# Kernel tuning notes

Hardware: AMD Instinct MI355X
Metric: run time of the kernel (lower is better)

The kernel has to match this reference:

```python
import jax, jax.numpy as jnp
import numpy as np
from jax import lax

VOCAB = 32000
EMBED = 300
HIDDEN = 1024
BATCH = 64
SEQLEN = 512


def setup_inputs() -> dict:
    key = jax.random.key(0)
    k1, k2, k3, k4 = jax.random.split(key, 4)
    seq = jax.random.randint(k1, (BATCH, SEQLEN), 0, VOCAB, dtype=jnp.int32)
    embedding_table = jax.random.normal(k2, (VOCAB, EMBED), dtype=jnp.float32) * 0.1
    # Keras LSTM params: kernel [E, 4H], recurrent_kernel [H, 4H], bias [4H]; gate order i,f,c,o
    kernel = jax.random.normal(k3, (EMBED, 4 * HIDDEN), dtype=jnp.float32) * (1.0 / np.sqrt(EMBED))
    recurrent_kernel = jax.random.normal(k4, (HIDDEN, 4 * HIDDEN), dtype=jnp.float32) * (1.0 / np.sqrt(HIDDEN))
    # Keras unit_forget_bias default: forget-gate bias = 1
    bias = jnp.concatenate([
        jnp.zeros((HIDDEN,), jnp.float32),
        jnp.ones((HIDDEN,), jnp.float32),
        jnp.zeros((2 * HIDDEN,), jnp.float32),
    ])
    return {"embedding_table": embedding_table, "kernel": kernel,
            "recurrent_kernel": recurrent_kernel, "bias": bias, "seq": seq}


def _masked_lstm(x, mask, kernel, recurrent_kernel, bias):
    # x: [B,T,E], mask: [B,T] bool. Returns final hidden state [B,H].
    B = x.shape[0]
    H = recurrent_kernel.shape[0]
    # precompute input projections for all steps: [T,B,4H]
    xz = jnp.einsum('bte,eg->tbg', x, kernel) + bias
    mask_t = mask.T  # [T,B]

    def step(carry, inp):
        h, c = carry
        zx, mt = inp  # zx [B,4H], mt [B]
        z = zx + h @ recurrent_kernel
        zi, zf, zg, zo = jnp.split(z, 4, axis=-1)
        i = jax.nn.sigmoid(zi)
        f = jax.nn.sigmoid(zf)
        g = jnp.tanh(zg)
        o = jax.nn.sigmoid(zo)
        c_new = f * c + i * g
        h_new = o * jnp.tanh(c_new)
        m = mt[:, None]
        h = jnp.where(m, h_new, h)
        c = jnp.where(m, c_new, c)
        return (h, c), None

    h0 = jnp.zeros((B, H), x.dtype)
    c0 = jnp.zeros((B, H), x.dtype)
    (h, _), _ = lax.scan(step, (h0, c0), (xz, mask_t))
    return h


def reference(embedding_table, kernel, recurrent_kernel, bias, seq):
    x = embedding_table[seq]          # [B,T,E] embedding lookup
    mask = seq != 0                   # mask_zero=True: token id 0 is padding
    return _masked_lstm(x, mask, kernel, recurrent_kernel, bias)
```

## Files before the change

### kernel.cpp

```cpp
#include <hip/hip_runtime.h>

#define TT 512
#define BB 64
#define EE 300
#define HH 1024
#define GG 4096
#define NSLOT 33

typedef _Float16 f16x8 __attribute__((ext_vector_type(8)));
typedef float f32x4 __attribute__((ext_vector_type(4)));


__device__ __forceinline__ float sigmf(float x) {
    return __fdividef(1.0f, 1.0f + __expf(-x));
}
__device__ __forceinline__ float tanhsf(float x) {
    float e = __expf(-2.0f * fabsf(x));
    float r = __fdividef(1.0f - e, 1.0f + e);
    return copysignf(r, x);
}

__global__ void mask_kernel(const int* __restrict__ seq, float* __restrict__ maskf) {
    int idx = blockIdx.x * 256 + threadIdx.x;
    int t = idx >> 6, b = idx & 63;
    maskf[idx] = (seq[b * TT + t] != 0) ? 1.0f : 0.0f;
}

__global__ __launch_bounds__(256)
void xgather_kernel(const float* __restrict__ emb, const int* __restrict__ seq,
                    _Float16* __restrict__ xA) {
    __shared__ float xrow[64 * 305];
    const int t = blockIdx.x, tid = threadIdx.x;
    const int r = tid >> 2, sub = tid & 3;
    const int row = seq[r * TT + t];
    for (int e = sub; e < EE; e += 4)
        xrow[r * 305 + e] = emb[row * EE + e];
    __syncthreads();
    unsigned int* dst = (unsigned int*)(xA + (size_t)t * 20480);
    for (int idx = tid; idx < 10240; idx += 256) {
        int el = idx << 1;
        int j = el & 7, b = (el >> 3) & 63, quad = (el >> 9) & 3, kb = el >> 11;
        int e = (kb << 5) + (quad << 3) + j;
        union { _Float16 h[2]; unsigned int u; } pk;
        pk.h[0] = (e < EE)     ? (_Float16)xrow[b * 305 + e]     : (_Float16)0.f;
        pk.h[1] = (e + 1 < EE) ? (_Float16)xrow[b * 305 + e + 1] : (_Float16)0.f;
        dst[idx] = pk.u;
    }
}

__global__ __launch_bounds__(512, 2)
void lstm_kernel(const _Float16* __restrict__ xA, const float* __restrict__ rk,
                 const float* __restrict__ wk, const float* __restrict__ bias,
                 const float* __restrict__ maskf, _Float16* __restrict__ hbuf,
                 unsigned int* __restrict__ flags, float* __restrict__ out) {
    __shared__ _Float16 RbL[16384];
    __shared__ _Float16 WbL[5120];
    __shared__ float zb[8704];
    __shared__ float cs[2048];
    __shared__ _Float16 hshh[256];
    const int tid = threadIdx.x;
    const int lane = tid & 63;
    const int w = tid >> 6;
    const int p = blockIdx.x;
    const int p4 = p << 2;
    const int cc = lane & 15, quad = lane >> 4;

    for (int i = tid; i < 16384; i += 512) {
        int k = i >> 4, c = i & 15;
        float v = rk[k * GG + ((c >> 2) << 10) + p4 + (c & 3)];
        RbL[((k >> 5) << 9) + (((k >> 3) & 3) << 7) + (c << 3) + (k & 7)] = (_Float16)v;
    }
    for (int i = tid; i < 5120; i += 512) {
        int e = i >> 4, c = i & 15;
        float v = (e < EE) ? wk[e * GG + ((c >> 2) << 10) + p4 + (c & 3)] : 0.f;
        WbL[((e >> 5) << 9) + (((e >> 3) & 3) << 7) + (c << 3) + (e & 7)] = (_Float16)v;
    }
    if (tid < 256) cs[tid] = 0.f;
    float bb[4];
    if (w < 4) {
#pragma unroll
        for (int gt = 0; gt < 4; ++gt)
            bb[gt] = bias[(gt << 10) + p4 + w];
    }
    int slot = 0, nslot = 1;
    float hown = 0.0f;
    const int fidx = (w << 5) + (lane & 31);
    const f16x8* RbH = (const f16x8*)RbL;
    const f16x8* WbH = (const f16x8*)WbL;
    __syncthreads();

    for (int t = 0; t < TT; ++t) {
        float m = maskf[(t << 6) + lane];
        f32x4 acc[4];
#pragma unroll
        for (int mt = 0; mt < 4; ++mt) acc[mt] = (f32x4){0.f, 0.f, 0.f, 0.f};

        const f16x8* xA8 = (const f16x8*)(xA + (size_t)t * 20480);
        {
            int kb = w;
            f16x8 bf = WbH[(kb << 6) + (quad << 4) + cc];
#pragma unroll
            for (int mt = 0; mt < 4; ++mt) {
                f16x8 af = xA8[(kb << 8) + (quad << 6) + (mt << 4) + cc];
                acc[mt] = __builtin_amdgcn_mfma_f32_16x16x32_f16(af, bf, acc[mt], 0, 0, 0);
            }
        }
        if (w < 2) {
            int kb = 8 + w;
            f16x8 bf = WbH[(kb << 6) + (quad << 4) + cc];
#pragma unroll
            for (int mt = 0; mt < 4; ++mt) {
                f16x8 af = xA8[(kb << 8) + (quad << 6) + (mt << 4) + cc];
                acc[mt] = __builtin_amdgcn_mfma_f32_16x16x32_f16(af, bf, acc[mt], 0, 0, 0);
            }
        }

        if (t > 0) {
            unsigned int tgt = (unsigned int)t;
            while (!__all((int)(__hip_atomic_load(flags + fidx, __ATOMIC_RELAXED,
                                                  __HIP_MEMORY_SCOPE_AGENT) >= tgt)))
                __builtin_amdgcn_s_sleep(1);
        }
        __builtin_amdgcn_sched_barrier(0);

        const f16x8* hA8 = (const f16x8*)(hbuf + (size_t)slot * 65536);
#pragma unroll
        for (int kc = 0; kc < 4; ++kc) {
            int kb = (w << 2) + kc;
            f16x8 bf = RbH[(kb << 6) + (quad << 4) + cc];
#pragma unroll
            for (int mt = 0; mt < 4; ++mt) {
                f16x8 af = hA8[(kb << 8) + (quad << 6) + (mt << 4) + cc];
                acc[mt] = __builtin_amdgcn_mfma_f32_16x16x32_f16(af, bf, acc[mt], 0, 0, 0);
            }
        }
#pragma unroll
        for (int mt = 0; mt < 4; ++mt)
            *(f32x4*)(zb + ((w << 4) + cc) * 68 + (mt << 4) + (quad << 2)) = acc[mt];
        __syncthreads();
        if (w < 4) {
            float z[4];
#pragma unroll
            for (int gt = 0; gt < 4; ++gt) {
                int c = (gt << 2) + w;
                float s = bb[gt];
#pragma unroll
                for (int wp = 0; wp < 8; ++wp) s += zb[((wp << 4) + c) * 68 + lane];
                z[gt] = s;
            }
            float fi = sigmf(z[0]);
            float ff = sigmf(z[1]);
            float fg = tanhsf(z[2]);
            float fo = sigmf(z[3]);
            float co = cs[(w << 6) + lane];
            float cn = fmaf(ff, co, fi * fg);
            cn = fmaf(m, cn - co, co);
            cs[(w << 6) + lane] = cn;
            float hc = fo * tanhsf(cn);
            hown = fmaf(m, hc - hown, hown);
            hshh[(lane << 2) + w] = (_Float16)hown;
        }
        __syncthreads();
        if (tid < 64) {
            unsigned long long hv = ((const unsigned long long*)hshh)[lane];
            size_t el = (size_t)nslot * 65536 + ((size_t)(p >> 3) << 11) +
                        ((size_t)((p >> 1) & 3) << 9) + (lane << 3) + ((p & 1) << 2);
            __hip_atomic_store((unsigned long long*)(hbuf + el), hv,
                               __ATOMIC_RELAXED, __HIP_MEMORY_SCOPE_AGENT);
        }
        __syncthreads();
        if (tid == 0)
            __hip_atomic_store(flags + p, (unsigned int)(t + 1),
                               __ATOMIC_RELAXED, __HIP_MEMORY_SCOPE_AGENT);
        slot = nslot;
        nslot = (nslot + 1 == NSLOT) ? 0 : nslot + 1;
    }
    if (w < 4) zb[(w << 6) + lane] = hown;
    __syncthreads();
    if (tid < 64) {
        float4 v = make_float4(zb[tid], zb[64 + tid], zb[128 + tid], zb[192 + tid]);
        *(float4*)(out + tid * HH + p4) = v;
    }
}

extern "C" void kernel_launch(void* const* d_in, const int* in_sizes, int n_in,
                              void* d_out, int out_size, void* d_ws, size_t ws_size,
                              hipStream_t stream) {
    const float* emb  = (const float*)d_in[0];
    const float* wk   = (const float*)d_in[1];
    const float* rk   = (const float*)d_in[2];
    const float* bias = (const float*)d_in[3];
    const int*   seq  = (const int*)d_in[4];
    float* out = (float*)d_out;
    char* ws = (char*)d_ws;

    const size_t off_hbuf = 1024;
    const size_t off_mask = off_hbuf + (size_t)NSLOT * 131072;
    const size_t off_xA   = off_mask + 131072;
    unsigned int* flags = (unsigned int*)ws;
    _Float16* hbuf  = (_Float16*)(ws + off_hbuf);
    float*    maskf = (float*)(ws + off_mask);
    _Float16* xA    = (_Float16*)(ws + off_xA);

    hipMemsetAsync(ws, 0, off_hbuf + 131072, stream);
    mask_kernel<<<128, 256, 0, stream>>>(seq, maskf);
    xgather_kernel<<<TT, 256, 0, stream>>>(emb, seq, xA);
    lstm_kernel<<<256, 512, 0, stream>>>(xA, rk, wk, bias, maskf, hbuf, flags, out);
}
```

Baseline: 1.880 ms.

## Warp-specialize LSTM step into producer MFMA warps and consumer gate warp pipelined per batch group

Each step is split across waves. Seven waves compute MFMA partial sums for one 16-row batch group at a time, and one dedicated wave reduces them, applies the gate nonlinearities and publishes h. Block-wide __syncthreads are replaced by per-wave progress counters in LDS and a double-buffered z buffer, so gate math for one group overlaps the matmul for the next. The recurrent and input weight fragments are hoisted into registers, and the xA and hbuf layouts are changed to group-major. A dummy padding shared array, touched only behind an impossible pointer check, forces LDS usage, which looks aimed at limiting occupancy. The change adds spin-wait complexity and the risk of ordering bugs.

```diff
diff --git a/kernel.cpp b/kernel.cpp
--- a/kernel.cpp
+++ b/kernel.cpp
@@ -39,11 +39,13 @@
     unsigned int* dst = (unsigned int*)(xA + (size_t)t * 20480);
     for (int idx = tid; idx < 10240; idx += 256) {
         int el = idx << 1;
-        int j = el & 7, b = (el >> 3) & 63, quad = (el >> 9) & 3, kb = el >> 11;
+        int j = el & 7, b = (el >> 3) & 15, quad = (el >> 7) & 3, r2 = el >> 9;
+        int g = r2 / 10, kb = r2 - g * 10;
         int e = (kb << 5) + (quad << 3) + j;
+        int bg = (g << 4) + b;
         union { _Float16 h[2]; unsigned int u; } pk;
-        pk.h[0] = (e < EE)     ? (_Float16)xrow[b * 305 + e]     : (_Float16)0.f;
-        pk.h[1] = (e + 1 < EE) ? (_Float16)xrow[b * 305 + e + 1] : (_Float16)0.f;
+        pk.h[0] = (e < EE)     ? (_Float16)xrow[bg * 305 + e]     : (_Float16)0.f;
+        pk.h[1] = (e + 1 < EE) ? (_Float16)xrow[bg * 305 + e + 1] : (_Float16)0.f;
         dst[idx] = pk.u;
     }
 }
@@ -55,9 +57,12 @@
                  unsigned int* __restrict__ flags, float* __restrict__ out) {
     __shared__ _Float16 RbL[16384];
     __shared__ _Float16 WbL[5120];
-    __shared__ float zb[8704];
-    __shared__ float cs[2048];
-    __shared__ _Float16 hshh[256];
+    __shared__ float zb[4480];
+    __shared__ float cs[256];
+    __shared__ __align__(8) _Float16 hsh[64];
+    __shared__ unsigned int prog[8];
+    __shared__ unsigned int rel;
+    __shared__ float padf[6200];
     const int tid = threadIdx.x;
     const int lane = tid & 63;
     const int w = tid >> 6;
@@ -76,110 +81,125 @@
         WbL[((e >> 5) << 9) + (((e >> 3) & 3) << 7) + (c << 3) + (e & 7)] = (_Float16)v;
     }
     if (tid < 256) cs[tid] = 0.f;
-    float bb[4];
-    if (w < 4) {
-#pragma unroll
-        for (int gt = 0; gt < 4; ++gt)
-            bb[gt] = bias[(gt << 10) + p4 + w];
-    }
-    int slot = 0, nslot = 1;
-    float hown = 0.0f;
-    const int fidx = (w << 5) + (lane & 31);
-    const f16x8* RbH = (const f16x8*)RbL;
-    const f16x8* WbH = (const f16x8*)WbL;
+    if (tid < 8) prog[tid] = (tid == 7) ? 0xFFFFFFFFu : 0u;
+    if (tid == 0) rel = 0u;
     __syncthreads();
-
-    for (int t = 0; t < TT; ++t) {
-        float m = maskf[(t << 6) + lane];
-        f32x4 acc[4];
-#pragma unroll
-        for (int mt = 0; mt < 4; ++mt) acc[mt] = (f32x4){0.f, 0.f, 0.f, 0.f};
-
-        const f16x8* xA8 = (const f16x8*)(xA + (size_t)t * 20480);
-        {
-            int kb = w;
-            f16x8 bf = WbH[(kb << 6) + (quad << 4) + cc];
-#pragma unroll
-            for (int mt = 0; mt < 4; ++mt) {
-                f16x8 af = xA8[(kb << 8) + (quad << 6) + (mt << 4) + cc];
-                acc[mt] = __builtin_amdgcn_mfma_f32_16x16x32_f16(af, bf, acc[mt], 0, 0, 0);
+    if ((size_t)out == 1) { padf[tid] = cs[0]; out[0] = padf[tid]; }
+
+    if (w == 0) {
+        const int uu = lane >> 4, b = lane & 15;
+        float bb0 = bias[p4 + uu], bb1 = bias[1024 + p4 + uu];
+        float bb2 = bias[2048 + p4 + uu], bb3 = bias[3072 + p4 + uu];
+        float hw[4] = {0.f, 0.f, 0.f, 0.f};
+        const size_t puboff = ((((size_t)(p >> 3) << 2) + ((p >> 1) & 3)) << 7)
+                              + ((size_t)lane << 3) + ((size_t)(p & 1) << 2);
+        for (int t = 0; t < TT; ++t) {
+            _Float16* hb = hbuf + (size_t)((t + 1) % NSLOT) * 65536;
+#pragma unroll
+            for (int g = 0; g < 4; ++g) {
+                const int id = (t << 2) + g;
+                while (!__all((int)(__hip_atomic_load(prog + (lane & 7), __ATOMIC_ACQUIRE,
+                                                      __HIP_MEMORY_SCOPE_WORKGROUP)
+                                    >= (unsigned)(id + 1))))
+                    __builtin_amdgcn_s_sleep(0);
+                __builtin_amdgcn_sched_barrier(0);
+                const float* zr = zb + (id & 1) * 2240;
+                float z0 = bb0, z1 = bb1, z2 = bb2, z3 = bb3;
+#pragma unroll
+                for (int wp = 0; wp < 7; ++wp) {
+                    const float* zw = zr + (wp << 4) * 20;
+                    z0 += zw[uu * 20 + b];
+                    z1 += zw[(4 + uu) * 20 + b];
+                    z2 += zw[(8 + uu) * 20 + b];
+                    z3 += zw[(12 + uu) * 20 + b];
+                }
+                if (lane == 0)
+                    __hip_atomic_store(&rel, (unsigned)(id + 1), __ATOMIC_RELEASE,
+                                       __HIP_MEMORY_SCOPE_WORKGROUP);
+                float m = maskf[(t << 6) + (g << 4) + b];
+                float fi = sigmf(z0);
+                float ff = sigmf(z1);
+                float fg = tanhsf(z2);
+                float fo = sigmf(z3);
+                float co = cs[(g << 6) + lane];
+                float cn = fmaf(ff, co, fi * fg);
+                cn = fmaf(m, cn - co, co);
+                cs[(g << 6) + lane] = cn;
+                float hc = fo * tanhsf(cn);
+                hw[g] = fmaf(m, hc - hw[g], hw[g]);
+                hsh[(b << 2) + uu] = (_Float16)hw[g];
+                if (lane < 16) {
+                    unsigned long long hv = ((const unsigned long long*)hsh)[lane];
+                    __hip_atomic_store((unsigned long long*)(hb + ((size_t)g << 14) + puboff),
+                                       hv, __ATOMIC_RELAXED, __HIP_MEMORY_SCOPE_AGENT);
+                }
+            }
+            __asm__ volatile("s_waitcnt vmcnt(0)" ::: "memory");
+            if (lane == 0)
+                __hip_atomic_store(flags + p, (unsigned)(t + 1),
+                                   __ATOMIC_RELAXED, __HIP_MEMORY_SCOPE_AGENT);
+        }
+#pragma unroll
+        for (int g = 0; g < 4; ++g)
+            out[(((g << 4) + b) << 10) + p4 + uu] = hw[g];
+    } else {
+        const int wi = w - 1;
+        const int rec0 = (wi < 4) ? wi * 5 : 20 + ((wi - 4) << 2);
+        const int nrec = (wi < 4) ? 5 : 4;
+        const int xw0  = (wi < 4) ? wi : 4 + ((wi - 4) << 1);
+        const int nxw  = (wi < 4) ? 1 : 2;
+        f16x8 bfr[5], bfx[2];
+#pragma unroll
+        for (int r = 0; r < 5; ++r) if (r < nrec)
+            bfr[r] = *(const f16x8*)(RbL + ((rec0 + r) << 9) + (quad << 7) + (cc << 3));
+#pragma unroll
+        for (int xi = 0; xi < 2; ++xi) if (xi < nxw)
+            bfx[xi] = *(const f16x8*)(WbL + ((xw0 + xi) << 9) + (quad << 7) + (cc << 3));
+        const int nprod = nrec << 3;
+        const int fl = (rec0 << 3) + ((lane < nprod) ? lane : nprod - 1);
+
+        for (int t = 0; t < TT; ++t) {
+            f32x4 acc[4];
+#pragma unroll
+            for (int g = 0; g < 4; ++g) acc[g] = (f32x4){0.f, 0.f, 0.f, 0.f};
+            const f16x8* xt8 = (const f16x8*)(xA + (size_t)t * 20480);
+#pragma unroll
+            for (int xi = 0; xi < 2; ++xi) if (xi < nxw) {
+                const int kb = xw0 + xi;
+#pragma unroll
+                for (int g = 0; g < 4; ++g) {
+                    f16x8 af = xt8[g * 640 + (kb << 6) + (quad << 4) + cc];
+                    acc[g] = __builtin_amdgcn_mfma_f32_16x16x32_f16(af, bfx[xi], acc[g], 0, 0, 0);
+                }
+            }
+            unsigned tgt = (unsigned)t;
+            while (!__all((int)(__hip_atomic_load(flags + fl, __ATOMIC_RELAXED,
+                                                  __HIP_MEMORY_SCOPE_AGENT) >= tgt)))
+                __builtin_amdgcn_s_sleep(1);
+            __builtin_amdgcn_sched_barrier(0);
+            const f16x8* h8 = (const f16x8*)(hbuf + (size_t)(t % NSLOT) * 65536);
+#pragma unroll
+            for (int g = 0; g < 4; ++g) {
+                const int id = (t << 2) + g;
+                if (id >= 2) {
+                    while (__hip_atomic_load(&rel, __ATOMIC_ACQUIRE,
+                                             __HIP_MEMORY_SCOPE_WORKGROUP) < (unsigned)(id - 1))
+                        __builtin_amdgcn_s_sleep(0);
+                }
+                __builtin_amdgcn_sched_barrier(0);
+                const f16x8* hg = h8 + ((size_t)g << 11);
+#pragma unroll
+                for (int r = 0; r < 5; ++r) if (r < nrec) {
+                    const int kb = rec0 + r;
+                    f16x8 af = hg[(kb << 6) + (quad << 4) + cc];
+                    acc[g] = __builtin_amdgcn_mfma_f32_16x16x32_f16(af, bfr[r], acc[g], 0, 0, 0);
+                }
+                *(f32x4*)(zb + (id & 1) * 2240 + ((wi << 4) + cc) * 20 + (quad << 2)) = acc[g];
+                if (lane == 0)
+                    __hip_atomic_store(prog + wi, (unsigned)(id + 1), __ATOMIC_RELEASE,
+                                       __HIP_MEMORY_SCOPE_WORKGROUP);
             }
         }
-        if (w < 2) {
-            int kb = 8 + w;
-            f16x8 bf = WbH[(kb << 6) + (quad << 4) + cc];
-#pragma unroll
-            for (int mt = 0; mt < 4; ++mt) {
-                f16x8 af = xA8[(kb << 8) + (quad << 6) + (mt << 4) + cc];
-                acc[mt] = __builtin_amdgcn_mfma_f32_16x16x32_f16(af, bf, acc[mt], 0, 0, 0);
-            }
-        }
-
-        if (t > 0) {
-            unsigned int tgt = (unsigned int)t;
-            while (!__all((int)(__hip_atomic_load(flags + fidx, __ATOMIC_RELAXED,
-                                                  __HIP_MEMORY_SCOPE_AGENT) >= tgt)))
-                __builtin_amdgcn_s_sleep(1);
-        }
-        __builtin_amdgcn_sched_barrier(0);
-
-        const f16x8* hA8 = (const f16x8*)(hbuf + (size_t)slot * 65536);
-#pragma unroll
-        for (int kc = 0; kc < 4; ++kc) {
-            int kb = (w << 2) + kc;
-            f16x8 bf = RbH[(kb << 6) + (quad << 4) + cc];
-#pragma unroll
-            for (int mt = 0; mt < 4; ++mt) {
-                f16x8 af = hA8[(kb << 8) + (quad << 6) + (mt << 4) + cc];
-                acc[mt] = __builtin_amdgcn_mfma_f32_16x16x32_f16(af, bf, acc[mt], 0, 0, 0);
-            }
-        }
-#pragma unroll
-        for (int mt = 0; mt < 4; ++mt)
-            *(f32x4*)(zb + ((w << 4) + cc) * 68 + (mt << 4) + (quad << 2)) = acc[mt];
-        __syncthreads();
-        if (w < 4) {
-            float z[4];
-#pragma unroll
-            for (int gt = 0; gt < 4; ++gt) {
-                int c = (gt << 2) + w;
-                float s = bb[gt];
-#pragma unroll
-                for (int wp = 0; wp < 8; ++wp) s += zb[((wp << 4) + c) * 68 + lane];
-                z[gt] = s;
-            }
-            float fi = sigmf(z[0]);
-            float ff = sigmf(z[1]);
-            float fg = tanhsf(z[2]);
-            float fo = sigmf(z[3]);
-            float co = cs[(w << 6) + lane];
-            float cn = fmaf(ff, co, fi * fg);
-            cn = fmaf(m, cn - co, co);
-            cs[(w << 6) + lane] = cn;
-            float hc = fo * tanhsf(cn);
-            hown = fmaf(m, hc - hown, hown);
-            hshh[(lane << 2) + w] = (_Float16)hown;
-        }
-        __syncthreads();
-        if (tid < 64) {
-            unsigned long long hv = ((const unsigned long long*)hshh)[lane];
-            size_t el = (size_t)nslot * 65536 + ((size_t)(p >> 3) << 11) +
-                        ((size_t)((p >> 1) & 3) << 9) + (lane << 3) + ((p & 1) << 2);
-            __hip_atomic_store((unsigned long long*)(hbuf + el), hv,
-                               __ATOMIC_RELAXED, __HIP_MEMORY_SCOPE_AGENT);
-        }
-        __syncthreads();
-        if (tid == 0)
-            __hip_atomic_store(flags + p, (unsigned int)(t + 1),
-                               __ATOMIC_RELAXED, __HIP_MEMORY_SCOPE_AGENT);
-        slot = nslot;
-        nslot = (nslot + 1 == NSLOT) ? 0 : nslot + 1;
-    }
-    if (w < 4) zb[(w << 6) + lane] = hown;
-    __syncthreads();
-    if (tid < 64) {
-        float4 v = make_float4(zb[tid], zb[64 + tid], zb[128 + tid], zb[192 + tid]);
-        *(float4*)(out + tid * HH + p4) = v;
     }
 }
 
```

New measurement: 4.471 ms. 138% more time.

## Split LSTM recurrence by batch group per wave, keep weights in registers

Applied to the files above, without the earlier changes.

The persistent LSTM kernel now uses 256 threads per block. Each of the four waves owns a 16-row batch group and computes the whole K reduction for it, instead of splitting K across eight waves and reducing through shared memory. Recurrent and input weight fragments are held in registers. Per-wave flags, h publication and a register-resident cell state remove the block-wide __syncthreads barriers from each timestep. The xA and hbuf layouts are reordered so each batch group's rows are contiguous, and a padding array limits the kernel to one block per CU. In exchange, each wave issues more serial MFMAs and register pressure rises.

```diff
diff --git a/kernel.cpp b/kernel.cpp
--- a/kernel.cpp
+++ b/kernel.cpp
@@ -39,148 +39,139 @@
     unsigned int* dst = (unsigned int*)(xA + (size_t)t * 20480);
     for (int idx = tid; idx < 10240; idx += 256) {
         int el = idx << 1;
-        int j = el & 7, b = (el >> 3) & 63, quad = (el >> 9) & 3, kb = el >> 11;
+        int j = el & 7, b = (el >> 3) & 15, quad = (el >> 7) & 3, r2 = el >> 9;
+        int g = r2 / 10, kb = r2 - g * 10;
         int e = (kb << 5) + (quad << 3) + j;
+        int bg = (g << 4) + b;
         union { _Float16 h[2]; unsigned int u; } pk;
-        pk.h[0] = (e < EE)     ? (_Float16)xrow[b * 305 + e]     : (_Float16)0.f;
-        pk.h[1] = (e + 1 < EE) ? (_Float16)xrow[b * 305 + e + 1] : (_Float16)0.f;
+        pk.h[0] = (e < EE)     ? (_Float16)xrow[bg * 305 + e]     : (_Float16)0.f;
+        pk.h[1] = (e + 1 < EE) ? (_Float16)xrow[bg * 305 + e + 1] : (_Float16)0.f;
         dst[idx] = pk.u;
     }
 }
 
-__global__ __launch_bounds__(512, 2)
+__global__ __launch_bounds__(256, 1)
 void lstm_kernel(const _Float16* __restrict__ xA, const float* __restrict__ rk,
                  const float* __restrict__ wk, const float* __restrict__ bias,
                  const float* __restrict__ maskf, _Float16* __restrict__ hbuf,
                  unsigned int* __restrict__ flags, float* __restrict__ out) {
     __shared__ _Float16 RbL[16384];
     __shared__ _Float16 WbL[5120];
-    __shared__ float zb[8704];
-    __shared__ float cs[2048];
-    __shared__ _Float16 hshh[256];
+    __shared__ float zsc[4][272];
+    __shared__ __align__(8) _Float16 zh[4][64];
+    __shared__ float padf[16000];
     const int tid = threadIdx.x;
     const int lane = tid & 63;
-    const int w = tid >> 6;
+    const int g = tid >> 6;
     const int p = blockIdx.x;
     const int p4 = p << 2;
     const int cc = lane & 15, quad = lane >> 4;
 
-    for (int i = tid; i < 16384; i += 512) {
+    ((volatile float*)padf)[tid] = 0.f;
+
+    for (int i = tid; i < 16384; i += 256) {
         int k = i >> 4, c = i & 15;
         float v = rk[k * GG + ((c >> 2) << 10) + p4 + (c & 3)];
         RbL[((k >> 5) << 9) + (((k >> 3) & 3) << 7) + (c << 3) + (k & 7)] = (_Float16)v;
     }
-    for (int i = tid; i < 5120; i += 512) {
+    for (int i = tid; i < 5120; i += 256) {
         int e = i >> 4, c = i & 15;
         float v = (e < EE) ? wk[e * GG + ((c >> 2) << 10) + p4 + (c & 3)] : 0.f;
         WbL[((e >> 5) << 9) + (((e >> 3) & 3) << 7) + (c << 3) + (e & 7)] = (_Float16)v;
     }
-    if (tid < 256) cs[tid] = 0.f;
-    float bb[4];
-    if (w < 4) {
-#pragma unroll
-        for (int gt = 0; gt < 4; ++gt)
-            bb[gt] = bias[(gt << 10) + p4 + w];
-    }
+    __syncthreads();
+
+    f16x8 bR[32], bW[10];
+#pragma unroll
+    for (int kb = 0; kb < 32; ++kb)
+        bR[kb] = *(const f16x8*)(RbL + (kb << 9) + (quad << 7) + (cc << 3));
+#pragma unroll
+    for (int kb = 0; kb < 10; ++kb)
+        bW[kb] = *(const f16x8*)(WbL + (kb << 9) + (quad << 7) + (cc << 3));
+
+    const float bb0 = bias[p4 + quad];
+    const float bb1 = bias[1024 + p4 + quad];
+    const float bb2 = bias[2048 + p4 + quad];
+    const float bb3 = bias[3072 + p4 + quad];
+    float c_st = 0.f, hw = 0.f;
     int slot = 0, nslot = 1;
-    float hown = 0.0f;
-    const int fidx = (w << 5) + (lane & 31);
-    const f16x8* RbH = (const f16x8*)RbL;
-    const f16x8* WbH = (const f16x8*)WbL;
-    __syncthreads();
+    const unsigned int* fg = flags + (g << 8);
+    const size_t pub_base = ((size_t)(p >> 3) << 7) + ((size_t)((p >> 1) & 3) << 5) +
+                            ((size_t)lane << 1) + (size_t)(p & 1) + ((size_t)g << 12);
 
     for (int t = 0; t < TT; ++t) {
-        float m = maskf[(t << 6) + lane];
         f32x4 acc[4];
 #pragma unroll
-        for (int mt = 0; mt < 4; ++mt) acc[mt] = (f32x4){0.f, 0.f, 0.f, 0.f};
-
-        const f16x8* xA8 = (const f16x8*)(xA + (size_t)t * 20480);
+        for (int i = 0; i < 4; ++i) acc[i] = (f32x4){0.f, 0.f, 0.f, 0.f};
+
+        const f16x8* xt8 = (const f16x8*)(xA + (size_t)t * 20480) + g * 640;
+#pragma unroll
+        for (int kb = 0; kb < 10; ++kb) {
+            f16x8 af = xt8[(kb << 6) + (quad << 4) + cc];
+            acc[kb & 3] = __builtin_amdgcn_mfma_f32_16x16x32_f16(af, bW[kb], acc[kb & 3], 0, 0, 0);
+        }
+        float m = maskf[(t << 6) + (g << 4) + cc];
+
         {
-            int kb = w;
-            f16x8 bf = WbH[(kb << 6) + (quad << 4) + cc];
-#pragma unroll
-            for (int mt = 0; mt < 4; ++mt) {
-                f16x8 af = xA8[(kb << 8) + (quad << 6) + (mt << 4) + cc];
-                acc[mt] = __builtin_amdgcn_mfma_f32_16x16x32_f16(af, bf, acc[mt], 0, 0, 0);
+            unsigned tgt = (unsigned)t;
+            for (;;) {
+                unsigned f0 = __hip_atomic_load(fg + lane,       __ATOMIC_RELAXED, __HIP_MEMORY_SCOPE_AGENT);
+                unsigned f1 = __hip_atomic_load(fg + 64 + lane,  __ATOMIC_RELAXED, __HIP_MEMORY_SCOPE_AGENT);
+                unsigned f2 = __hip_atomic_load(fg + 128 + lane, __ATOMIC_RELAXED, __HIP_MEMORY_SCOPE_AGENT);
+                unsigned f3 = __hip_atomic_load(fg + 192 + lane, __ATOMIC_RELAXED, __HIP_MEMORY_SCOPE_AGENT);
+                unsigned mn = min(min(f0, f1), min(f2, f3));
+                if (__all((int)(mn >= tgt))) break;
+                __builtin_amdgcn_s_sleep(1);
             }
         }
-        if (w < 2) {
-            int kb = 8 + w;
-            f16x8 bf = WbH[(kb << 6) + (quad << 4) + cc];
-#pragma unroll
-            for (int mt = 0; mt < 4; ++mt) {
-                f16x8 af = xA8[(kb << 8) + (quad << 6) + (mt << 4) + cc];
-                acc[mt] = __builtin_amdgcn_mfma_f32_16x16x32_f16(af, bf, acc[mt], 0, 0, 0);
+        __builtin_amdgcn_sched_barrier(0);
+
+        const f16x8* hp8 = (const f16x8*)hbuf + (size_t)slot * 8192 + ((size_t)g << 11);
+        f16x8 hv[8];
+#pragma unroll
+        for (int i = 0; i < 8; ++i) hv[i] = hp8[(i << 6) + (quad << 4) + cc];
+#pragma unroll
+        for (int g8 = 0; g8 < 4; ++g8) {
+#pragma unroll
+            for (int j = 0; j < 8; ++j) {
+                f16x8 cur = hv[j];
+                const int kb = (g8 << 3) + j;
+                if (g8 < 3) hv[j] = hp8[((kb + 8) << 6) + (quad << 4) + cc];
+                acc[kb & 3] = __builtin_amdgcn_mfma_f32_16x16x32_f16(cur, bR[kb], acc[kb & 3], 0, 0, 0);
             }
         }
-
-        if (t > 0) {
-            unsigned int tgt = (unsigned int)t;
-            while (!__all((int)(__hip_atomic_load(flags + fidx, __ATOMIC_RELAXED,
-                                                  __HIP_MEMORY_SCOPE_AGENT) >= tgt)))
-                __builtin_amdgcn_s_sleep(1);
-        }
-        __builtin_amdgcn_sched_barrier(0);
-
-        const f16x8* hA8 = (const f16x8*)(hbuf + (size_t)slot * 65536);
-#pragma unroll
-        for (int kc = 0; kc < 4; ++kc) {
-            int kb = (w << 2) + kc;
-            f16x8 bf = RbH[(kb << 6) + (quad << 4) + cc];
-#pragma unroll
-            for (int mt = 0; mt < 4; ++mt) {
-                f16x8 af = hA8[(kb << 8) + (quad << 6) + (mt << 4) + cc];
-                acc[mt] = __builtin_amdgcn_mfma_f32_16x16x32_f16(af, bf, acc[mt], 0, 0, 0);
-            }
-        }
-#pragma unroll
-        for (int mt = 0; mt < 4; ++mt)
-            *(f32x4*)(zb + ((w << 4) + cc) * 68 + (mt << 4) + (quad << 2)) = acc[mt];
-        __syncthreads();
-        if (w < 4) {
-            float z[4];
-#pragma unroll
-            for (int gt = 0; gt < 4; ++gt) {
-                int c = (gt << 2) + w;
-                float s = bb[gt];
-#pragma unroll
-                for (int wp = 0; wp < 8; ++wp) s += zb[((wp << 4) + c) * 68 + lane];
-                z[gt] = s;
-            }
-            float fi = sigmf(z[0]);
-            float ff = sigmf(z[1]);
-            float fg = tanhsf(z[2]);
-            float fo = sigmf(z[3]);
-            float co = cs[(w << 6) + lane];
-            float cn = fmaf(ff, co, fi * fg);
-            cn = fmaf(m, cn - co, co);
-            cs[(w << 6) + lane] = cn;
-            float hc = fo * tanhsf(cn);
-            hown = fmaf(m, hc - hown, hown);
-            hshh[(lane << 2) + w] = (_Float16)hown;
-        }
-        __syncthreads();
-        if (tid < 64) {
-            unsigned long long hv = ((const unsigned long long*)hshh)[lane];
-            size_t el = (size_t)nslot * 65536 + ((size_t)(p >> 3) << 11) +
-                        ((size_t)((p >> 1) & 3) << 9) + (lane << 3) + ((p & 1) << 2);
-            __hip_atomic_store((unsigned long long*)(hbuf + el), hv,
-                               __ATOMIC_RELAXED, __HIP_MEMORY_SCOPE_AGENT);
-        }
-        __syncthreads();
-        if (tid == 0)
-            __hip_atomic_store(flags + p, (unsigned int)(t + 1),
+        f32x4 s = (acc[0] + acc[1]) + (acc[2] + acc[3]);
+
+#pragma unroll
+        for (int i = 0; i < 4; ++i)
+            zsc[g][((quad << 2) + i) * 17 + cc] = s[i];
+        float z0 = zsc[g][cc * 17 + quad]      + bb0;
+        float z1 = zsc[g][cc * 17 + 4 + quad]  + bb1;
+        float z2 = zsc[g][cc * 17 + 8 + quad]  + bb2;
+        float z3 = zsc[g][cc * 17 + 12 + quad] + bb3;
+        float fi = sigmf(z0);
+        float ff = sigmf(z1);
+        float fgv = tanhsf(z2);
+        float fo = sigmf(z3);
+        float cn = fmaf(ff, c_st, fi * fgv);
+        cn = fmaf(m, cn - c_st, c_st);
+        c_st = cn;
+        float hc = fo * tanhsf(cn);
+        hw = fmaf(m, hc - hw, hw);
+        zh[g][(cc << 2) + quad] = (_Float16)hw;
+        if (lane < 16) {
+            unsigned long long hv8 = ((const unsigned long long*)(&zh[g][0]))[lane];
+            __hip_atomic_store((unsigned long long*)hbuf + (size_t)nslot * 16384 + pub_base,
+                               hv8, __ATOMIC_RELAXED, __HIP_MEMORY_SCOPE_AGENT);
+        }
+        __asm__ volatile("s_waitcnt vmcnt(0)" ::: "memory");
+        if (lane == 0)
+            __hip_atomic_store(flags + (g << 8) + p, (unsigned)(t + 1),
                                __ATOMIC_RELAXED, __HIP_MEMORY_SCOPE_AGENT);
         slot = nslot;
         nslot = (nslot + 1 == NSLOT) ? 0 : nslot + 1;
     }
-    if (w < 4) zb[(w << 6) + lane] = hown;
-    __syncthreads();
-    if (tid < 64) {
-        float4 v = make_float4(zb[tid], zb[64 + tid], zb[128 + tid], zb[192 + tid]);
-        *(float4*)(out + tid * HH + p4) = v;
-    }
+    out[(((g << 4) + cc) << 10) + p4 + quad] = hw;
 }
 
 extern "C" void kernel_launch(void* const* d_in, const int* in_sizes, int n_in,
@@ -194,7 +185,7 @@
     float* out = (float*)d_out;
     char* ws = (char*)d_ws;
 
-    const size_t off_hbuf = 1024;
+    const size_t off_hbuf = 4096;
     const size_t off_mask = off_hbuf + (size_t)NSLOT * 131072;
     const size_t off_xA   = off_mask + 131072;
     unsigned int* flags = (unsigned int*)ws;
@@ -205,5 +196,5 @@
     hipMemsetAsync(ws, 0, off_hbuf + 131072, stream);
     mask_kernel<<<128, 256, 0, stream>>>(seq, maskf);
     xgather_kernel<<<TT, 256, 0, stream>>>(emb, seq, xA);
-    lstm_kernel<<<256, 512, 0, stream>>>(xA, rk, wk, bias, maskf, hbuf, flags, out);
-}
+    lstm_kernel<<<256, 256, 0, stream>>>(xA, rk, wk, bias, maskf, hbuf, flags, out);
+}
```

New measurement: 2.634 ms. 1.4x slower.

## Split LSTM block into producer MFMA waves and dedicated gate-update wave with double-buffered partials

Applied to the files above, without the earlier changes.

Wave 0 becomes a dedicated consumer that sums partial gate pre-activations from a double-buffered shared array, applies the LSTM cell update for all four hidden units in registers, and publishes h and the step flag. The other seven waves keep their recurrent and input weight fragments in registers and compute MFMA partials for the next step while wave 0 works on the current one. The intent is to overlap gate math and publication with the next step's matmul and to cut per-step barriers. Each step now uses one barrier instead of three. The trade-off is uneven MFMA work across seven waves, a single wave doing all the elementwise math, extra LDS padding, and a larger flag region.

```diff
diff --git a/kernel.cpp b/kernel.cpp
--- a/kernel.cpp
+++ b/kernel.cpp
@@ -53,11 +53,11 @@
                  const float* __restrict__ wk, const float* __restrict__ bias,
                  const float* __restrict__ maskf, _Float16* __restrict__ hbuf,
                  unsigned int* __restrict__ flags, float* __restrict__ out) {
-    __shared__ _Float16 RbL[16384];
-    __shared__ _Float16 WbL[5120];
-    __shared__ float zb[8704];
-    __shared__ float cs[2048];
-    __shared__ _Float16 hshh[256];
+    __shared__ union {
+        struct { _Float16 Rb[16384]; _Float16 Wb[5120]; } st;
+        float zbl[2][7][1280];
+    } U;
+    __shared__ float padL[3200];
     const int tid = threadIdx.x;
     const int lane = tid & 63;
     const int w = tid >> 6;
@@ -65,121 +65,135 @@
     const int p4 = p << 2;
     const int cc = lane & 15, quad = lane >> 4;
 
+    ((volatile float*)padL)[tid] = 0.f;
+
     for (int i = tid; i < 16384; i += 512) {
         int k = i >> 4, c = i & 15;
         float v = rk[k * GG + ((c >> 2) << 10) + p4 + (c & 3)];
-        RbL[((k >> 5) << 9) + (((k >> 3) & 3) << 7) + (c << 3) + (k & 7)] = (_Float16)v;
+        U.st.Rb[((k >> 5) << 9) + (((k >> 3) & 3) << 7) + (c << 3) + (k & 7)] = (_Float16)v;
     }
     for (int i = tid; i < 5120; i += 512) {
         int e = i >> 4, c = i & 15;
         float v = (e < EE) ? wk[e * GG + ((c >> 2) << 10) + p4 + (c & 3)] : 0.f;
-        WbL[((e >> 5) << 9) + (((e >> 3) & 3) << 7) + (c << 3) + (e & 7)] = (_Float16)v;
-    }
-    if (tid < 256) cs[tid] = 0.f;
-    float bb[4];
-    if (w < 4) {
-#pragma unroll
-        for (int gt = 0; gt < 4; ++gt)
-            bb[gt] = bias[(gt << 10) + p4 + w];
-    }
-    int slot = 0, nslot = 1;
-    float hown = 0.0f;
-    const int fidx = (w << 5) + (lane & 31);
-    const f16x8* RbH = (const f16x8*)RbL;
-    const f16x8* WbH = (const f16x8*)WbL;
+        U.st.Wb[((e >> 5) << 9) + (((e >> 3) & 3) << 7) + (c << 3) + (e & 7)] = (_Float16)v;
+    }
     __syncthreads();
 
-    for (int t = 0; t < TT; ++t) {
-        float m = maskf[(t << 6) + lane];
-        f32x4 acc[4];
-#pragma unroll
-        for (int mt = 0; mt < 4; ++mt) acc[mt] = (f32x4){0.f, 0.f, 0.f, 0.f};
-
-        const f16x8* xA8 = (const f16x8*)(xA + (size_t)t * 20480);
-        {
-            int kb = w;
-            f16x8 bf = WbH[(kb << 6) + (quad << 4) + cc];
-#pragma unroll
-            for (int mt = 0; mt < 4; ++mt) {
-                f16x8 af = xA8[(kb << 8) + (quad << 6) + (mt << 4) + cc];
-                acc[mt] = __builtin_amdgcn_mfma_f32_16x16x32_f16(af, bf, acc[mt], 0, 0, 0);
-            }
+    if (w == 0) {
+        float bbi[4], bbf[4], bbg[4], bbo[4];
+#pragma unroll
+        for (int u = 0; u < 4; ++u) {
+            bbi[u] = bias[p4 + u];
+            bbf[u] = bias[1024 + p4 + u];
+            bbg[u] = bias[2048 + p4 + u];
+            bbo[u] = bias[3072 + p4 + u];
         }
-        if (w < 2) {
-            int kb = 8 + w;
-            f16x8 bf = WbH[(kb << 6) + (quad << 4) + cc];
-#pragma unroll
-            for (int mt = 0; mt < 4; ++mt) {
-                f16x8 af = xA8[(kb << 8) + (quad << 6) + (mt << 4) + cc];
-                acc[mt] = __builtin_amdgcn_mfma_f32_16x16x32_f16(af, bf, acc[mt], 0, 0, 0);
-            }
+        float cst[4] = {0.f, 0.f, 0.f, 0.f};
+        float hwv[4] = {0.f, 0.f, 0.f, 0.f};
+        const size_t pub_base = ((size_t)(p >> 3) << 9) + ((size_t)((p >> 1) & 3) << 7)
+                                + ((size_t)lane << 1) + (size_t)(p & 1);
+        __syncthreads();
+        int pslot = 1;
+        for (int t = 0; t < TT; ++t) {
+            __syncthreads();
+            float m = maskf[(t << 6) + lane];
+            const float* zr = &U.zbl[t & 1][0][0] + lane * 20;
+            float sacc[16];
+#pragma unroll
+            for (int q4 = 0; q4 < 4; ++q4) {
+                f32x4 v = *(const f32x4*)(zr + (q4 << 2));
+#pragma unroll
+                for (int wi2 = 1; wi2 < 7; ++wi2)
+                    v += *(const f32x4*)(zr + wi2 * 1280 + (q4 << 2));
+                sacc[(q4 << 2) + 0] = v[0]; sacc[(q4 << 2) + 1] = v[1];
+                sacc[(q4 << 2) + 2] = v[2]; sacc[(q4 << 2) + 3] = v[3];
+            }
+            union { _Float16 hp[4]; unsigned long long u64; } pk;
+#pragma unroll
+            for (int u = 0; u < 4; ++u) {
+                float zi = sacc[u] + bbi[u];
+                float zf = sacc[4 + u] + bbf[u];
+                float zg = sacc[8 + u] + bbg[u];
+                float zo = sacc[12 + u] + bbo[u];
+                float fi = sigmf(zi);
+                float ff = sigmf(zf);
+                float fg = tanhsf(zg);
+                float fo = sigmf(zo);
+                float cn = fmaf(ff, cst[u], fi * fg);
+                cn = fmaf(m, cn - cst[u], cst[u]);
+                cst[u] = cn;
+                float hc = fo * tanhsf(cn);
+                hwv[u] = fmaf(m, hc - hwv[u], hwv[u]);
+                pk.hp[u] = (_Float16)hwv[u];
+            }
+            __hip_atomic_store((unsigned long long*)hbuf + (size_t)pslot * 16384 + pub_base,
+                               pk.u64, __ATOMIC_RELAXED, __HIP_MEMORY_SCOPE_AGENT);
+            __asm__ volatile("s_waitcnt vmcnt(0)" ::: "memory");
+            if (lane == 0)
+                __hip_atomic_store(flags + p, (unsigned)(t + 1),
+                                   __ATOMIC_RELAXED, __HIP_MEMORY_SCOPE_AGENT);
+            pslot = (pslot + 1 == NSLOT) ? 0 : pslot + 1;
         }
-
-        if (t > 0) {
-            unsigned int tgt = (unsigned int)t;
-            while (!__all((int)(__hip_atomic_load(flags + fidx, __ATOMIC_RELAXED,
-                                                  __HIP_MEMORY_SCOPE_AGENT) >= tgt)))
-                __builtin_amdgcn_s_sleep(1);
+        *(float4*)(out + lane * HH + p4) =
+            make_float4(hwv[0], hwv[1], hwv[2], hwv[3]);
+    } else {
+        const int wi = w - 1;
+        const int rec0 = (wi < 4) ? wi * 5 : 20 + ((wi - 4) << 2);
+        const int nrec = (wi < 4) ? 5 : 4;
+        const int xw0  = (wi < 4) ? wi : 4 + ((wi - 4) << 1);
+        const int nxw  = (wi < 4) ? 1 : 2;
+        f16x8 bR[5], bW[2];
+#pragma unroll
+        for (int r = 0; r < 5; ++r) if (r < nrec)
+            bR[r] = *(const f16x8*)(U.st.Rb + ((rec0 + r) << 9) + (quad << 7) + (cc << 3));
+#pragma unroll
+        for (int xi = 0; xi < 2; ++xi) if (xi < nxw)
+            bW[xi] = *(const f16x8*)(U.st.Wb + ((xw0 + xi) << 9) + (quad << 7) + (cc << 3));
+        const int nprod = nrec << 3;
+        const int fl = (rec0 << 3) + ((lane < nprod) ? lane : nprod - 1);
+        __syncthreads();
+
+        int ps = 0;
+        for (int s = 0; s < TT; ++s) {
+            f32x4 acc[4];
+#pragma unroll
+            for (int mt = 0; mt < 4; ++mt) acc[mt] = (f32x4){0.f, 0.f, 0.f, 0.f};
+            const f16x8* xt8 = (const f16x8*)(xA + (size_t)s * 20480);
+#pragma unroll
+            for (int xi = 0; xi < 2; ++xi) if (xi < nxw) {
+                const int kb = xw0 + xi;
+#pragma unroll
+                for (int mt = 0; mt < 4; ++mt) {
+                    f16x8 af = xt8[(kb << 8) + (quad << 6) + (mt << 4) + cc];
+                    acc[mt] = __builtin_amdgcn_mfma_f32_16x16x32_f16(af, bW[xi], acc[mt], 0, 0, 0);
+                }
+            }
+            {
+                unsigned tgt = (unsigned)s;
+                while (!__all((int)(__hip_atomic_load(flags + fl, __ATOMIC_RELAXED,
+                                                      __HIP_MEMORY_SCOPE_AGENT) >= tgt)))
+                    __builtin_amdgcn_s_sleep(1);
+            }
+            __builtin_amdgcn_sched_barrier(0);
+            const f16x8* hp8 = (const f16x8*)hbuf + (size_t)ps * 8192;
+#pragma unroll
+            for (int r = 0; r < 5; ++r) if (r < nrec) {
+                const int kb = rec0 + r;
+#pragma unroll
+                for (int mt = 0; mt < 4; ++mt) {
+                    f16x8 af = hp8[(kb << 8) + (quad << 6) + (mt << 4) + cc];
+                    acc[mt] = __builtin_amdgcn_mfma_f32_16x16x32_f16(af, bR[r], acc[mt], 0, 0, 0);
+                }
+            }
+            float* zw = &U.zbl[s & 1][wi][0];
+#pragma unroll
+            for (int mt = 0; mt < 4; ++mt)
+#pragma unroll
+                for (int i = 0; i < 4; ++i)
+                    zw[((mt << 4) + (quad << 2) + i) * 20 + cc] = acc[mt][i];
+            ps = (ps + 1 == NSLOT) ? 0 : ps + 1;
+            __syncthreads();
         }
-        __builtin_amdgcn_sched_barrier(0);
-
-        const f16x8* hA8 = (const f16x8*)(hbuf + (size_t)slot * 65536);
-#pragma unroll
-        for (int kc = 0; kc < 4; ++kc) {
-            int kb = (w << 2) + kc;
-            f16x8 bf = RbH[(kb << 6) + (quad << 4) + cc];
-#pragma unroll
-            for (int mt = 0; mt < 4; ++mt) {
-                f16x8 af = hA8[(kb << 8) + (quad << 6) + (mt << 4) + cc];
-                acc[mt] = __builtin_amdgcn_mfma_f32_16x16x32_f16(af, bf, acc[mt], 0, 0, 0);
-            }
-        }
-#pragma unroll
-        for (int mt = 0; mt < 4; ++mt)
-            *(f32x4*)(zb + ((w << 4) + cc) * 68 + (mt << 4) + (quad << 2)) = acc[mt];
-        __syncthreads();
-        if (w < 4) {
-            float z[4];
-#pragma unroll
-            for (int gt = 0; gt < 4; ++gt) {
-                int c = (gt << 2) + w;
-                float s = bb[gt];
-#pragma unroll
-                for (int wp = 0; wp < 8; ++wp) s += zb[((wp << 4) + c) * 68 + lane];
-                z[gt] = s;
-            }
-            float fi = sigmf(z[0]);
-            float ff = sigmf(z[1]);
-            float fg = tanhsf(z[2]);
-            float fo = sigmf(z[3]);
-            float co = cs[(w << 6) + lane];
-            float cn = fmaf(ff, co, fi * fg);
-            cn = fmaf(m, cn - co, co);
-            cs[(w << 6) + lane] = cn;
-            float hc = fo * tanhsf(cn);
-            hown = fmaf(m, hc - hown, hown);
-            hshh[(lane << 2) + w] = (_Float16)hown;
-        }
-        __syncthreads();
-        if (tid < 64) {
-            unsigned long long hv = ((const unsigned long long*)hshh)[lane];
-            size_t el = (size_t)nslot * 65536 + ((size_t)(p >> 3) << 11) +
-                        ((size_t)((p >> 1) & 3) << 9) + (lane << 3) + ((p & 1) << 2);
-            __hip_atomic_store((unsigned long long*)(hbuf + el), hv,
-                               __ATOMIC_RELAXED, __HIP_MEMORY_SCOPE_AGENT);
-        }
-        __syncthreads();
-        if (tid == 0)
-            __hip_atomic_store(flags + p, (unsigned int)(t + 1),
-                               __ATOMIC_RELAXED, __HIP_MEMORY_SCOPE_AGENT);
-        slot = nslot;
-        nslot = (nslot + 1 == NSLOT) ? 0 : nslot + 1;
-    }
-    if (w < 4) zb[(w << 6) + lane] = hown;
-    __syncthreads();
-    if (tid < 64) {
-        float4 v = make_float4(zb[tid], zb[64 + tid], zb[128 + tid], zb[192 + tid]);
-        *(float4*)(out + tid * HH + p4) = v;
     }
 }
 
@@ -194,7 +208,7 @@
     float* out = (float*)d_out;
     char* ws = (char*)d_ws;
 
-    const size_t off_hbuf = 1024;
+    const size_t off_hbuf = 4096;
     const size_t off_mask = off_hbuf + (size_t)NSLOT * 131072;
     const size_t off_xA   = off_mask + 131072;
     unsigned int* flags = (unsigned int*)ws;
```

After: 3.934 ms. +109.3%, slower.
